# Performance work log

Measured on AMD Instinct MI355X. Metric: run time of the kernel, lower is better.

The kernel has to match this reference:

```python
import jax, jax.numpy as jnp
import numpy as np

B, N, T_FULL, T, KS, FEAT = 32, 360, 512, 64, 8, 8
NLAYERS = 3   # DCGRU layers
GLAYERS = 4   # bidirectional GRU layers in GruKRegion


def _gru_layer(x, Wih, Whh, bih, bhh, reverse):
    # x: [M, Tg, in] -> [M, Tg, H]; PyTorch GRU gate order (r, z, n)
    M = x.shape[0]
    Hh = Whh.shape[1]
    xp = jnp.einsum('mti,gi->mtg', x, Wih) + bih  # precompute input projections
    if reverse:
        xp = xp[:, ::-1]

    def step(h, xg):
        gh = jnp.einsum('mh,gh->mg', h, Whh) + bhh
        xr, xz, xn = jnp.split(xg, 3, -1)
        hr, hz, hn = jnp.split(gh, 3, -1)
        r = jax.nn.sigmoid(xr + hr)
        z = jax.nn.sigmoid(xz + hz)
        n = jnp.tanh(xn + r * hn)
        hnew = (1.0 - z) * n + z * h
        return hnew, hnew

    _, hs = jax.lax.scan(step, jnp.zeros((M, Hh), x.dtype), jnp.swapaxes(xp, 0, 1))
    hs = jnp.swapaxes(hs, 0, 1)
    if reverse:
        hs = hs[:, ::-1]
    return hs


def _dcgru_cell(x, h, adj, gw, gb, cw, cb):
    # x, h: [B, N] (rnn_units = 1); adj: [B, N, N]; max_diffusion_step = 2
    def gconv(inp, st, W, bias):
        x0 = jnp.stack([inp, st], axis=-1)                     # [B,N,2]
        x1 = jnp.einsum('bnm,bmc->bnc', adj, x0)
        x2 = 2.0 * jnp.einsum('bnm,bmc->bnc', adj, x1) - x0    # Chebyshev recurrence
        # torch layout: [B,N,C,num_matrices] flattened channel-major
        xc = jnp.stack([x0, x1, x2], axis=-1).reshape(x0.shape[0], N, 6)
        return jnp.einsum('bnf,fo->bno', xc, W) + bias

    gates = jax.nn.sigmoid(gconv(x, h, gw, gb))                # [B,N,2]
    r, u = gates[..., 0], gates[..., 1]
    c = jnp.tanh(gconv(x, r * h, cw, cb)[..., 0])
    return u * h + (1.0 - u) * c


def _forward(full_seq, reconstruct_seq, node_feas, temperature,
             g0wih, g0whh, g0bih, g0bhh, gwih, gwhh, gbih, gbhh,
             l1w, l1b, l2w, l2b,
             enc_gw, enc_gb, enc_cw, enc_cb,
             dec_gw, dec_gb, dec_cw, dec_cb, proj_w, proj_b):
    b, n, tfull = full_seq.shape
    # ---- GruKRegion feature extractor ----
    x = full_seq.reshape(b * n, tfull // KS, KS)
    out = jnp.concatenate(
        [_gru_layer(x, g0wih[0], g0whh[0], g0bih[0], g0bhh[0], False),
         _gru_layer(x, g0wih[1], g0whh[1], g0bih[1], g0bhh[1], True)], axis=-1)
    for l in range(GLAYERS - 1):
        out = jnp.concatenate(
            [_gru_layer(out, gwih[l, 0], gwhh[l, 0], gbih[l, 0], gbhh[l, 0], False),
             _gru_layer(out, gwih[l, 1], gwhh[l, 1], gbih[l, 1], gbhh[l, 1], True)], axis=-1)
    feat = out[:, -1, :].reshape(b, n, 2 * KS)
    feat = jax.nn.leaky_relu(jnp.einsum('bnf,of->bno', feat, l1w) + l1b, 0.2)
    feat = jnp.einsum('bnf,of->bno', feat, l2w) + l2b          # [B,N,FEAT]
    # ---- Embed2GraphByProduct ----
    logits = jnp.einsum('bjk,bpk->bjp', feat, feat)            # [B,N,N]
    # ---- hard gumbel softmax ----
    U = jax.random.uniform(jax.random.key(42), logits.shape, logits.dtype)
    g = -jnp.log(-jnp.log(U + 1e-10) + 1e-10)
    y_soft = jax.nn.softmax((logits + g) / temperature, axis=-1)
    y_hard = jax.nn.one_hot(jnp.argmax(y_soft, -1), n, dtype=y_soft.dtype)
    adj = y_soft + jax.lax.stop_gradient(y_hard - y_soft)
    adj = jnp.where(jnp.eye(n, dtype=bool), 0.0, adj)          # zero diagonal
    # (original computes a random-walk matrix then discards it; skipped)
    # ---- encoder: scan over time, 3 stacked DCGRU layers ----
    seq = jnp.transpose(reconstruct_seq, (2, 0, 1))            # [T,B,N]

    def enc_step(hid, xt):
        o = xt
        new = []
        for l in range(NLAYERS):
            hnew = _dcgru_cell(o, hid[l], adj, enc_gw[l], enc_gb[l], enc_cw[l], enc_cb[l])
            new.append(hnew)
            o = hnew
        return jnp.stack(new), None

    hid, _ = jax.lax.scan(enc_step, jnp.zeros((NLAYERS, b, n), seq.dtype), seq)

    def dec_step(carry, _):
        hidc, inp = carry
        o = inp
        new = []
        for l in range(NLAYERS):
            hnew = _dcgru_cell(o, hidc[l], adj, dec_gw[l], dec_gb[l], dec_cw[l], dec_cb[l])
            new.append(hnew)
            o = hnew
        proj = o * proj_w[0, 0] + proj_b[0]                    # Linear(1,1)
        return (jnp.stack(new), proj), proj

    _, outs = jax.lax.scan(dec_step, (hid, jnp.zeros((b, n), seq.dtype)), None, length=T)
    return jnp.transpose(outs, (1, 2, 0))                      # [B,N,T]


def setup_inputs():
    key = jax.random.key(0)
    ks = jax.random.split(key, 24)
    s = 0.2
    p = lambda k, sh: jax.random.normal(k, sh, jnp.float32) * s
    return dict(
        full_seq=jax.random.normal(ks[0], (B, N, T_FULL), jnp.float32),
        reconstruct_seq=jax.random.normal(ks[1], (B, N, T), jnp.float32),
        node_feas=jax.random.normal(ks[2], (B, N, KS), jnp.float32),
        temperature=jnp.ones((), jnp.float32),
        g0wih=p(ks[3], (2, 3 * KS, KS)), g0whh=p(ks[4], (2, 3 * KS, KS)),
        g0bih=p(ks[5], (2, 3 * KS)), g0bhh=p(ks[6], (2, 3 * KS)),
        gwih=p(ks[7], (GLAYERS - 1, 2, 3 * KS, 2 * KS)),
        gwhh=p(ks[8], (GLAYERS - 1, 2, 3 * KS, KS)),
        gbih=p(ks[9], (GLAYERS - 1, 2, 3 * KS)), gbhh=p(ks[10], (GLAYERS - 1, 2, 3 * KS)),
        l1w=p(ks[11], (KS, 2 * KS)), l1b=p(ks[12], (KS,)),
        l2w=p(ks[13], (FEAT, KS)), l2b=p(ks[14], (FEAT,)),
        enc_gw=p(ks[15], (NLAYERS, 6, 2)), enc_gb=jnp.ones((NLAYERS, 2), jnp.float32),
        enc_cw=p(ks[16], (NLAYERS, 6, 1)), enc_cb=jnp.zeros((NLAYERS, 1), jnp.float32),
        dec_gw=p(ks[17], (NLAYERS, 6, 2)), dec_gb=jnp.ones((NLAYERS, 2), jnp.float32),
        dec_cw=p(ks[18], (NLAYERS, 6, 1)), dec_cb=jnp.zeros((NLAYERS, 1), jnp.float32),
        proj_w=p(ks[19], (1, 1)), proj_b=jnp.zeros((1,), jnp.float32),
    )


def reference(full_seq, reconstruct_seq, node_feas, temperature,
              g0wih, g0whh, g0bih, g0bhh, gwih, gwhh, gbih, gbhh,
              l1w, l1b, l2w, l2b,
              enc_gw, enc_gb, enc_cw, enc_cb,
              dec_gw, dec_gb, dec_cw, dec_cb, proj_w, proj_b):
    return _forward(full_seq, reconstruct_seq, node_feas, temperature,
                    g0wih, g0whh, g0bih, g0bhh, gwih, gwhh, gbih, gbhh,
                    l1w, l1b, l2w, l2b,
                    enc_gw, enc_gb, enc_cw, enc_cb,
                    dec_gw, dec_gb, dec_cw, dec_cb, proj_w, proj_b)
```

## Files before the change

### kernel.cpp

```cpp
#include <hip/hip_runtime.h>
#include <math.h>

#define M_SEQ 11520
#define NNODE 360
#define NB    32
#define TT    64

__device__ __forceinline__ float fsigd(float x)  { return 1.0f / (1.0f + __expf(-x)); }
__device__ __forceinline__ float ftanhd(float x) { return 1.0f - 2.0f / (__expf(2.0f * x) + 1.0f); }

__device__ __forceinline__ void lds_barrier()
{
    asm volatile("s_waitcnt lgkmcnt(0)" ::: "memory");
    __builtin_amdgcn_sched_barrier(0);
    __builtin_amdgcn_s_barrier();
    __builtin_amdgcn_sched_barrier(0);
}

__device__ __forceinline__ unsigned rotl32(unsigned x, int n) { return (x << n) | (x >> (32 - n)); }

__device__ __forceinline__ void tf2x32(unsigned& x0, unsigned& x1)
{
    const unsigned k0 = 0u, k1 = 42u, k2 = 0u ^ 42u ^ 0x1BD11BDAu;
    x0 += k0; x1 += k1;
#define R4(a,b,c,d) \
    x0 += x1; x1 = rotl32(x1,a); x1 ^= x0; \
    x0 += x1; x1 = rotl32(x1,b); x1 ^= x0; \
    x0 += x1; x1 = rotl32(x1,c); x1 ^= x0; \
    x0 += x1; x1 = rotl32(x1,d); x1 ^= x0;
    R4(13,15,26,6)   x0 += k1; x1 += k2 + 1u;
    R4(17,29,16,24)  x0 += k2; x1 += k0 + 2u;
    R4(13,15,26,6)   x0 += k0; x1 += k1 + 3u;
    R4(17,29,16,24)  x0 += k1; x1 += k2 + 4u;
    R4(13,15,26,6)   x0 += k2; x1 += k0 + 5u;
#undef R4
}

__device__ __forceinline__ float jax_uniform(unsigned idx)
{
    unsigned x0 = 0u, x1 = idx;
    tf2x32(x0, x1);
    unsigned bits = x0 ^ x1;
    return __uint_as_float((bits >> 9) | 0x3f800000u) - 1.0f;
}

template<int K>
__device__ __forceinline__ void swz_fma(float h, const float* w0, const float* w1,
                                        const float* w2, float& g0, float& g1, float& g2)
{
    float hk = __int_as_float(
        __builtin_amdgcn_ds_swizzle(__float_as_int(h), (K << 5) | 0x18));
    g0 += hk * w0[K];
    g1 += hk * w1[K];
    g2 += hk * w2[K];
    if constexpr (K < 7)
        swz_fma<K + 1>(h, w0, w1, w2, g0, g1, g2);
}

template<int I>
__device__ __forceinline__ void ldx(float* __restrict__ xv, const float* __restrict__ p)
{
    const float4* p4 = reinterpret_cast<const float4*>(p);
#pragma unroll
    for (int q = 0; q < I / 4; ++q) {
        float4 f = p4[q];
        xv[4*q] = f.x; xv[4*q+1] = f.y; xv[4*q+2] = f.z; xv[4*q+3] = f.w;
    }
}

template<int I>
__device__ __forceinline__ void xgates(const float* __restrict__ xv,
    const float* wx0, const float* wx1, const float* wx2,
    float bx0, float bx1, float bx2, float& xr, float& xz, float& xn)
{
    xr = bx0; xz = bx1; xn = bx2;
#pragma unroll
    for (int k = 0; k < I; ++k) {
        xr += xv[k] * wx0[k];
        xz += xv[k] * wx1[k];
        xn += xv[k] * wx2[k];
    }
}

__device__ __forceinline__ float hstep(float h, float xr, float xz, float xn,
    const float* w0, const float* w1, const float* w2,
    float bh0, float bh1, float bh2)
{
    float gh0 = bh0, gh1 = bh1, gh2 = bh2;
    swz_fma<0>(h, w0, w1, w2, gh0, gh1, gh2);
    float r  = fsigd(xr + gh0);
    float z  = fsigd(xz + gh1);
    float nn = ftanhd(xn + r * gh2);
    return (1.f - z) * nn + z * h;
}

template<int I, bool LASTONLY>
__global__ __launch_bounds__(256) void gru_fused(
    const float* __restrict__ x,
    const float* __restrict__ wih,
    const float* __restrict__ whh,
    const float* __restrict__ bih,
    const float* __restrict__ bhh,
    float* __restrict__ out)
{
    const int tid = blockIdx.x * 256 + threadIdx.x;
    const int j   = tid & 7;
    const int md  = tid >> 3;
    if (md >= M_SEQ * 2) return;
    const int m = md >> 1, dir = md & 1;

    float wx0[I], wx1[I], wx2[I];
    const float* WI = wih + dir * 24 * I;
#pragma unroll
    for (int k = 0; k < I; ++k) {
        wx0[k] = WI[j * I + k];
        wx1[k] = WI[(8 + j) * I + k];
        wx2[k] = WI[(16 + j) * I + k];
    }
    float w0[8], w1[8], w2[8];
    const float* WH = whh + dir * 192;
#pragma unroll
    for (int k = 0; k < 8; ++k) {
        w0[k] = WH[j * 8 + k];
        w1[k] = WH[(8 + j) * 8 + k];
        w2[k] = WH[(16 + j) * 8 + k];
    }
    const float bx0 = bih[dir*24 + j], bx1 = bih[dir*24 + 8 + j], bx2 = bih[dir*24 + 16 + j];
    const float bh0 = bhh[dir*24 + j], bh1 = bhh[dir*24 + 8 + j], bh2 = bhh[dir*24 + 16 + j];

    const float* xm = x + (size_t)m * TT * I;
    float* om = out + (size_t)m * TT * 16 + dir * 8 + j;

    const int tstep = dir ? -1 : 1;
    const int tbase = dir ? TT - 1 : 0;

    float h = 0.f;
    float xva[I], xvb[I];
    ldx<I>(xva, xm + (tbase) * I);
    ldx<I>(xvb, xm + (tbase + tstep) * I);
    float cr, cz, cn;
    xgates<I>(xva, wx0, wx1, wx2, bx0, bx1, bx2, cr, cz, cn);

    for (int tt = 0; tt < TT; tt += 2) {
        const int t0 = tbase + tstep * tt;
        const int t1 = t0 + tstep;
        if (tt + 2 < TT) ldx<I>(xva, xm + (t0 + 2 * tstep) * I);
        float nr, nz, nn;
        xgates<I>(xvb, wx0, wx1, wx2, bx0, bx1, bx2, nr, nz, nn);
        h = hstep(h, cr, cz, cn, w0, w1, w2, bh0, bh1, bh2);
        if (!LASTONLY || t0 == TT - 1) om[t0 * 16] = h;
        if (tt + 3 < TT) ldx<I>(xvb, xm + (t0 + 3 * tstep) * I);
        h = hstep(h, nr, nz, nn, w0, w1, w2, bh0, bh1, bh2);
        if (!LASTONLY || t1 == TT - 1) om[t1 * 16] = h;
        xgates<I>(xva, wx0, wx1, wx2, bx0, bx1, bx2, cr, cz, cn);
    }
}

__global__ void feat_kernel(const float* __restrict__ gout,
                            const float* __restrict__ l1w, const float* __restrict__ l1b,
                            const float* __restrict__ l2w, const float* __restrict__ l2b,
                            float* __restrict__ feat)
{
    int m = blockIdx.x * blockDim.x + threadIdx.x;
    if (m >= M_SEQ) return;
    const float* xp = gout + (size_t)m * TT * 16 + (TT - 1) * 16;
    float xv[16];
#pragma unroll
    for (int i = 0; i < 16; ++i) xv[i] = xp[i];
    float h1[8];
#pragma unroll
    for (int o = 0; o < 8; ++o) {
        float a = 0.f;
#pragma unroll
        for (int f = 0; f < 16; ++f) a += xv[f] * l1w[o * 16 + f];
        a += l1b[o];
        h1[o] = (a >= 0.f) ? a : 0.2f * a;
    }
#pragma unroll
    for (int o = 0; o < 8; ++o) {
        float a = 0.f;
#pragma unroll
        for (int f = 0; f < 8; ++f) a += h1[f] * l2w[o * 8 + f];
        feat[(size_t)m * 8 + o] = a + l2b[o];
    }
}

__global__ void adj_kernel(const float* __restrict__ feat,
                           const float* __restrict__ tptr,
                           int* __restrict__ colp, float* __restrict__ vp)
{
    const int gw   = (blockIdx.x * blockDim.x + threadIdx.x) >> 6;
    const int lane = threadIdx.x & 63;
    if (gw >= NB * NNODE) return;
    const int b = gw / NNODE;
    const int n = gw - b * NNODE;
    const float T = tptr[0];
    const float* fb = feat + (size_t)b * NNODE * 8;
    float fn[8];
#pragma unroll
    for (int k = 0; k < 8; ++k) fn[k] = fb[(size_t)n * 8 + k];

    float sv[6];
    float mval = -3.0e38f; int midx = 1 << 30;
#pragma unroll
    for (int s = 0; s < 6; ++s) {
        int p = s * 64 + lane;
        float xs = -3.0e38f;
        if (p < NNODE) {
            const float* fp = fb + (size_t)p * 8;
            float d = 0.f;
#pragma unroll
            for (int k = 0; k < 8; ++k) d += fn[k] * fp[k];
            unsigned idx = (unsigned)gw * 360u + (unsigned)p;
            float u   = jax_uniform(idx);
            float gum = -logf(-logf(u + 1e-10f) + 1e-10f);
            xs = (d + gum) / T;
            if (xs > mval) { mval = xs; midx = p; }
        }
        sv[s] = xs;
    }
    for (int off = 32; off > 0; off >>= 1) {
        float ov = __shfl_xor(mval, off);
        int   oi = __shfl_xor(midx, off);
        if (ov > mval || (ov == mval && oi < midx)) { mval = ov; midx = oi; }
    }
    float ssum = 0.f;
#pragma unroll
    for (int s = 0; s < 6; ++s) {
        int p = s * 64 + lane;
        if (p < NNODE) ssum += expf(sv[s] - mval);
    }
    for (int off = 32; off > 0; off >>= 1) ssum += __shfl_xor(ssum, off);
    if (lane == 0) {
        float ys = 1.0f / ssum;
        float v  = ys + (1.0f - ys);
        if (midx == n) v = 0.0f;
        colp[gw] = midx;
        vp[gw]   = v;
    }
}

__device__ __forceinline__ void dc_layer(
    float o_own, float oa, float ob,
    float& hn, float ha, float hb,
    float v, float vv, int c1, int c2, bool act, int n,
    const float* __restrict__ W, float bgr, float bgu,
    const float* __restrict__ C, float cb,
    float* __restrict__ s_rh)
{
    float f1 = v * oa, f2 = vv * ob - o_own;
    float f4 = v * ha, f5 = vv * hb - hn;
    float r  = fsigd(o_own*W[0] + f1*W[2] + f2*W[4] + hn*W[6] + f4*W[8] + f5*W[10] + bgr);
    float rh = r * hn;
    if (act) s_rh[n] = rh;
    lds_barrier();
    float rha = s_rh[c1], rhb = s_rh[c2];
    float u  = fsigd(o_own*W[1] + f1*W[3] + f2*W[5] + hn*W[7] + f4*W[9] + f5*W[11] + bgu);
    float cnd = ftanhd(o_own*C[0] + f1*C[1] + f2*C[2] + rh*C[3]
                       + (v*rha)*C[4] + (vv*rhb - rh)*C[5] + cb);
    hn = u * hn + (1.f - u) * cnd;
}

__global__ __launch_bounds__(384, 1) void decode_kernel(
    const float* __restrict__ rec,
    const int*   __restrict__ colp, const float* __restrict__ vp,
    const float* __restrict__ egw, const float* __restrict__ egb,
    const float* __restrict__ ecw, const float* __restrict__ ecb,
    const float* __restrict__ dgw, const float* __restrict__ dgb,
    const float* __restrict__ dcw, const float* __restrict__ dcb,
    const float* __restrict__ pw,  const float* __restrict__ pb,
    float* __restrict__ outp)
{
    __shared__ float s_h[2][3][NNODE];
    __shared__ float s_x[2][NNODE];
    __shared__ float s_o[NNODE];
    __shared__ float s_rh[NNODE];
    __shared__ float s_v[NNODE];
    __shared__ int   s_c[NNODE];

    const int b = blockIdx.x;
    const int n = threadIdx.x;
    const bool act = n < NNODE;

    float inp0 = 0.f;
    if (act) {
        s_c[n] = colp[b * NNODE + n];
        s_v[n] = vp[b * NNODE + n];
        inp0   = rec[((size_t)b * NNODE + n) * TT + 0];
        s_h[0][0][n] = 0.f; s_h[0][1][n] = 0.f; s_h[0][2][n] = 0.f;
        s_x[0][n] = inp0;
    }
    __syncthreads();

    int c1 = 0, c2 = 0;
    float v = 0.f, vv = 0.f;
    if (act) {
        c1 = s_c[n];
        c2 = s_c[c1];
        v  = s_v[n];
        vv = 2.f * v * s_v[c1];
    }
    const float projw = pw[0], projb = pb[0];
    float hreg[3] = {0.f, 0.f, 0.f};

    float Wg[36], Bg[6], Wc[18], Cb[3];
#pragma unroll
    for (int k = 0; k < 36; ++k) Wg[k] = egw[k];
#pragma unroll
    for (int k = 0; k < 6;  ++k) Bg[k] = egb[k];
#pragma unroll
    for (int k = 0; k < 18; ++k) Wc[k] = ecw[k];
#pragma unroll
    for (int k = 0; k < 3;  ++k) Cb[k] = ecb[k];

    float o_own = inp0;
    int p = 0;
    for (int t = 0; t < TT; ++t) {
        float nx = (act && t + 1 < TT) ? rec[((size_t)b * NNODE + n) * TT + t + 1] : 0.f;
        float xa  = s_x[p][c1],    xb  = s_x[p][c2];
        float h0a = s_h[p][0][c1], h0b = s_h[p][0][c2];
        float h1a = s_h[p][1][c1], h1b = s_h[p][1][c2];
        float h2a = s_h[p][2][c1], h2b = s_h[p][2][c2];
        const int q = p ^ 1;
        dc_layer(o_own, xa, xb, hreg[0], h0a, h0b, v, vv, c1, c2, act, n,
                 Wg, Bg[0], Bg[1], Wc, Cb[0], s_rh);
        if (act) { s_h[q][0][n] = hreg[0]; s_o[n] = hreg[0]; }
        lds_barrier();
        float oa = s_o[c1], ob = s_o[c2];
        dc_layer(hreg[0], oa, ob, hreg[1], h1a, h1b, v, vv, c1, c2, act, n,
                 Wg + 12, Bg[2], Bg[3], Wc + 6, Cb[1], s_rh);
        if (act) { s_h[q][1][n] = hreg[1]; s_o[n] = hreg[1]; }
        lds_barrier();
        oa = s_o[c1]; ob = s_o[c2];
        dc_layer(hreg[1], oa, ob, hreg[2], h2a, h2b, v, vv, c1, c2, act, n,
                 Wg + 24, Bg[4], Bg[5], Wc + 12, Cb[2], s_rh);
        if (act) { s_h[q][2][n] = hreg[2]; s_x[q][n] = nx; }
        lds_barrier();
        o_own = nx; p = q;
    }

#pragma unroll
    for (int k = 0; k < 36; ++k) Wg[k] = dgw[k];
#pragma unroll
    for (int k = 0; k < 6;  ++k) Bg[k] = dgb[k];
#pragma unroll
    for (int k = 0; k < 18; ++k) Wc[k] = dcw[k];
#pragma unroll
    for (int k = 0; k < 3;  ++k) Cb[k] = dcb[k];

    float dinp = 0.f;
    for (int t = 0; t < TT; ++t) {
        float xa  = s_x[p][c1],    xb  = s_x[p][c2];
        float h0a = s_h[p][0][c1], h0b = s_h[p][0][c2];
        float h1a = s_h[p][1][c1], h1b = s_h[p][1][c2];
        float h2a = s_h[p][2][c1], h2b = s_h[p][2][c2];
        const int q = p ^ 1;
        dc_layer(dinp, xa, xb, hreg[0], h0a, h0b, v, vv, c1, c2, act, n,
                 Wg, Bg[0], Bg[1], Wc, Cb[0], s_rh);
        if (act) { s_h[q][0][n] = hreg[0]; s_o[n] = hreg[0]; }
        lds_barrier();
        float oa = s_o[c1], ob = s_o[c2];
        dc_layer(hreg[0], oa, ob, hreg[1], h1a, h1b, v, vv, c1, c2, act, n,
                 Wg + 12, Bg[2], Bg[3], Wc + 6, Cb[1], s_rh);
        if (act) { s_h[q][1][n] = hreg[1]; s_o[n] = hreg[1]; }
        lds_barrier();
        oa = s_o[c1]; ob = s_o[c2];
        dc_layer(hreg[1], oa, ob, hreg[2], h2a, h2b, v, vv, c1, c2, act, n,
                 Wg + 24, Bg[4], Bg[5], Wc + 12, Cb[2], s_rh);
        float proj = hreg[2] * projw + projb;
        if (act) {
            s_h[q][2][n] = hreg[2];
            s_x[q][n] = proj;
            outp[((size_t)b * NNODE + n) * TT + t] = proj;
        }
        lds_barrier();
        dinp = proj; p = q;
    }
}

extern "C" void kernel_launch(void* const* d_in, const int* in_sizes, int n_in,
                              void* d_out, int out_size, void* d_ws, size_t ws_size,
                              hipStream_t stream)
{
    (void)in_sizes; (void)n_in; (void)out_size; (void)ws_size;
    const float* full_seq = (const float*)d_in[0];
    const float* rec_seq  = (const float*)d_in[1];
    const float* temp     = (const float*)d_in[3];
    const float* g0wih    = (const float*)d_in[4];
    const float* g0whh    = (const float*)d_in[5];
    const float* g0bih    = (const float*)d_in[6];
    const float* g0bhh    = (const float*)d_in[7];
    const float* gwih     = (const float*)d_in[8];
    const float* gwhh     = (const float*)d_in[9];
    const float* gbih     = (const float*)d_in[10];
    const float* gbhh     = (const float*)d_in[11];
    const float* l1w      = (const float*)d_in[12];
    const float* l1b      = (const float*)d_in[13];
    const float* l2w      = (const float*)d_in[14];
    const float* l2b      = (const float*)d_in[15];
    const float* enc_gw   = (const float*)d_in[16];
    const float* enc_gb   = (const float*)d_in[17];
    const float* enc_cw   = (const float*)d_in[18];
    const float* enc_cb   = (const float*)d_in[19];
    const float* dec_gw   = (const float*)d_in[20];
    const float* dec_gb   = (const float*)d_in[21];
    const float* dec_cw   = (const float*)d_in[22];
    const float* dec_cb   = (const float*)d_in[23];
    const float* proj_w   = (const float*)d_in[24];
    const float* proj_b   = (const float*)d_in[25];
    float* outp = (float*)d_out;

    float* ws   = (float*)d_ws;
    float* feat = ws;
    float* vbuf = feat + (size_t)M_SEQ * 8;
    int*   cbuf = (int*)(vbuf + M_SEQ);
    float* bufA = (float*)(cbuf + M_SEQ);
    float* bufB = bufA + (size_t)M_SEQ * TT * 16;

    const int ggru = (M_SEQ * 2 * 8) / 256;
    gru_fused<8,false><<<ggru, 256, 0, stream>>>(full_seq, g0wih, g0whh, g0bih, g0bhh, bufA);
    gru_fused<16,false><<<ggru, 256, 0, stream>>>(bufA, gwih + 0 * 768, gwhh + 0 * 384,
                                                  gbih + 0 * 48, gbhh + 0 * 48, bufB);
    gru_fused<16,false><<<ggru, 256, 0, stream>>>(bufB, gwih + 1 * 768, gwhh + 1 * 384,
                                                  gbih + 1 * 48, gbhh + 1 * 48, bufA);
    gru_fused<16,true><<<ggru, 256, 0, stream>>>(bufA, gwih + 2 * 768, gwhh + 2 * 384,
                                                 gbih + 2 * 48, gbhh + 2 * 48, bufB);
    feat_kernel<<<M_SEQ / 256, 256, 0, stream>>>(bufB, l1w, l1b, l2w, l2b, feat);
    adj_kernel<<<(NB * NNODE) / 4, 256, 0, stream>>>(feat, temp, cbuf, vbuf);
    decode_kernel<<<NB, 384, 0, stream>>>(rec_seq, cbuf, vbuf,
                                          enc_gw, enc_gb, enc_cw, enc_cb,
                                          dec_gw, dec_gb, dec_cw, dec_cb,
                                          proj_w, proj_b, outp);
}
```

Measured before the change: 525.6 us.

## Wavefront-pipeline encoder DCGRU layers across two thread groups in decode kernel

The decode kernel now launches 768 threads per block and splits them into two groups of 384. During the encoder, group A computes layer 0 and most of layer 1 for step k while group B finishes layer 1 and computes layer 2 for step k-1. This skewed schedule shortens the serial chain of barrier-separated phases per timestep, since the encoder is latency-bound with only 32 blocks. It costs extra LDS buffers, a staged layer-1 handoff between the groups, and idle B threads during the decoder, which still runs sequentially.

```diff
diff --git a/kernel.cpp b/kernel.cpp
--- a/kernel.cpp
+++ b/kernel.cpp
@@ -241,6 +241,7 @@
 }
 
 __device__ __forceinline__ void dc_layer(
+    bool comp,
     float o_own, float oa, float ob,
     float& hn, float ha, float hb,
     float v, float vv, int c1, int c2, bool act, int n,
@@ -248,20 +249,25 @@
     const float* __restrict__ C, float cb,
     float* __restrict__ s_rh)
 {
-    float f1 = v * oa, f2 = vv * ob - o_own;
-    float f4 = v * ha, f5 = vv * hb - hn;
-    float r  = fsigd(o_own*W[0] + f1*W[2] + f2*W[4] + hn*W[6] + f4*W[8] + f5*W[10] + bgr);
-    float rh = r * hn;
-    if (act) s_rh[n] = rh;
+    float f1 = 0.f, f2 = 0.f, f4 = 0.f, f5 = 0.f, rh = 0.f;
+    if (comp) {
+        f1 = v * oa; f2 = vv * ob - o_own;
+        f4 = v * ha; f5 = vv * hb - hn;
+        float r = fsigd(o_own*W[0] + f1*W[2] + f2*W[4] + hn*W[6] + f4*W[8] + f5*W[10] + bgr);
+        rh = r * hn;
+        if (act) s_rh[n] = rh;
+    }
     lds_barrier();
-    float rha = s_rh[c1], rhb = s_rh[c2];
-    float u  = fsigd(o_own*W[1] + f1*W[3] + f2*W[5] + hn*W[7] + f4*W[9] + f5*W[11] + bgu);
-    float cnd = ftanhd(o_own*C[0] + f1*C[1] + f2*C[2] + rh*C[3]
-                       + (v*rha)*C[4] + (vv*rhb - rh)*C[5] + cb);
-    hn = u * hn + (1.f - u) * cnd;
-}
-
-__global__ __launch_bounds__(384, 1) void decode_kernel(
+    if (comp) {
+        float rha = s_rh[c1], rhb = s_rh[c2];
+        float u  = fsigd(o_own*W[1] + f1*W[3] + f2*W[5] + hn*W[7] + f4*W[9] + f5*W[11] + bgu);
+        float cnd = ftanhd(o_own*C[0] + f1*C[1] + f2*C[2] + rh*C[3]
+                           + (v*rha)*C[4] + (vv*rhb - rh)*C[5] + cb);
+        hn = u * hn + (1.f - u) * cnd;
+    }
+}
+
+__global__ __launch_bounds__(768, 1) void decode_kernel(
     const float* __restrict__ rec,
     const int*   __restrict__ colp, const float* __restrict__ vp,
     const float* __restrict__ egw, const float* __restrict__ egb,
@@ -272,36 +278,47 @@
     float* __restrict__ outp)
 {
     __shared__ float s_h[2][3][NNODE];
-    __shared__ float s_x[2][NNODE];
+    __shared__ float s_xe[2][NNODE];
+    __shared__ float s_r1[2][NNODE];
+    __shared__ float s_u1[2][NNODE];
+    __shared__ float s_c1[2][NNODE];
+    __shared__ float s_rh0[NNODE];
+    __shared__ float s_rh2[NNODE];
     __shared__ float s_o[NNODE];
-    __shared__ float s_rh[NNODE];
+    __shared__ float s_rhd[NNODE];
     __shared__ float s_v[NNODE];
     __shared__ int   s_c[NNODE];
 
-    const int b = blockIdx.x;
-    const int n = threadIdx.x;
-    const bool act = n < NNODE;
-
-    float inp0 = 0.f;
-    if (act) {
-        s_c[n] = colp[b * NNODE + n];
-        s_v[n] = vp[b * NNODE + n];
-        inp0   = rec[((size_t)b * NNODE + n) * TT + 0];
-        s_h[0][0][n] = 0.f; s_h[0][1][n] = 0.f; s_h[0][2][n] = 0.f;
-        s_x[0][n] = inp0;
+    const int  b    = blockIdx.x;
+    const int  tid  = threadIdx.x;
+    const bool isB  = tid >= 384;
+    const bool isA  = !isB;
+    const int  node = isB ? tid - 384 : tid;
+    const bool actN = node < NNODE;
+
+    const float* recb = rec + ((size_t)b * NNODE + node) * TT;
+
+    float o_own = 0.f, xq1 = 0.f;
+    if (isA && actN) {
+        s_c[node] = colp[b * NNODE + node];
+        s_v[node] = vp[b * NNODE + node];
+        o_own = recb[0];
+        xq1   = recb[1];
+        s_xe[0][node] = o_own;
+#pragma unroll
+        for (int l = 0; l < 3; ++l) { s_h[0][l][node] = 0.f; s_h[1][l][node] = 0.f; }
     }
     __syncthreads();
 
     int c1 = 0, c2 = 0;
     float v = 0.f, vv = 0.f;
-    if (act) {
-        c1 = s_c[n];
+    if (actN) {
+        c1 = s_c[node];
         c2 = s_c[c1];
-        v  = s_v[n];
+        v  = s_v[node];
         vv = 2.f * v * s_v[c1];
     }
     const float projw = pw[0], projb = pb[0];
-    float hreg[3] = {0.f, 0.f, 0.f};
 
     float Wg[36], Bg[6], Wc[18], Cb[3];
 #pragma unroll
@@ -313,65 +330,136 @@
 #pragma unroll
     for (int k = 0; k < 3;  ++k) Cb[k] = ecb[k];
 
-    float o_own = inp0;
+    float h0r = 0.f, h1r = 0.f, h2r = 0.f;
+
+    for (int k = 0; k <= TT; ++k) {
+        const int  pk = k & 1, qk = pk ^ 1;
+        const bool aAct = isA && actN && (k < TT);
+        const bool bAct = isB && actN && (k >= 1);
+        float nx2 = 0.f;
+        if (aAct && k + 2 < TT) nx2 = recb[k + 2];
+
+        float fA1=0.f, fA2=0.f, fA4=0.f, fA5=0.f, rhA=0.f;
+        if (isA) {
+            float xa  = s_xe[pk][c1],   xb  = s_xe[pk][c2];
+            float h0a = s_h[pk][0][c1], h0b = s_h[pk][0][c2];
+            fA1 = v * xa;  fA2 = vv * xb - o_own;
+            fA4 = v * h0a; fA5 = vv * h0b - h0r;
+            float rA = fsigd(o_own*Wg[0] + fA1*Wg[2] + fA2*Wg[4] + h0r*Wg[6]
+                             + fA4*Wg[8] + fA5*Wg[10] + Bg[0]);
+            rhA = rA * h0r;
+            if (aAct) s_rh0[node] = rhA;
+        } else {
+            float rh1o = s_r1[pk][node];
+            float rh1a = s_r1[pk][c1], rh1b = s_r1[pk][c2];
+            float u1v  = s_u1[pk][node], cp1v = s_c1[pk][node];
+            float cnd1 = ftanhd(cp1v + rh1o*Wc[9] + (v*rh1a)*Wc[10]
+                                + (vv*rh1b - rh1o)*Wc[11] + Cb[1]);
+            if (bAct) { h1r = u1v * h1r + (1.f - u1v) * cnd1; s_h[qk][1][node] = h1r; }
+        }
+        lds_barrier();
+
+        float fB1=0.f, fB2=0.f, fB4=0.f, fB5=0.f, rhB=0.f;
+        if (isA) {
+            float rh0a = s_rh0[c1], rh0b = s_rh0[c2];
+            float uA = fsigd(o_own*Wg[1] + fA1*Wg[3] + fA2*Wg[5] + h0r*Wg[7]
+                             + fA4*Wg[9] + fA5*Wg[11] + Bg[1]);
+            float cndA = ftanhd(o_own*Wc[0] + fA1*Wc[1] + fA2*Wc[2] + rhA*Wc[3]
+                                + (v*rh0a)*Wc[4] + (vv*rh0b - rhA)*Wc[5] + Cb[0]);
+            if (aAct) {
+                h0r = uA * h0r + (1.f - uA) * cndA;
+                s_h[qk][0][node] = h0r;
+                s_xe[qk][node]   = xq1;
+            }
+        } else {
+            float o2a = s_h[qk][1][c1], o2b = s_h[qk][1][c2];
+            float h2a = s_h[pk][2][c1], h2b = s_h[pk][2][c2];
+            fB1 = v * o2a; fB2 = vv * o2b - h1r;
+            fB4 = v * h2a; fB5 = vv * h2b - h2r;
+            float rB = fsigd(h1r*Wg[24] + fB1*Wg[26] + fB2*Wg[28] + h2r*Wg[30]
+                             + fB4*Wg[32] + fB5*Wg[34] + Bg[4]);
+            rhB = rB * h2r;
+            if (bAct) s_rh2[node] = rhB;
+        }
+        lds_barrier();
+
+        if (isA) {
+            float o1a = s_h[qk][0][c1], o1b = s_h[qk][0][c2];
+            float h1own = s_h[qk][1][node];
+            float h1a = s_h[qk][1][c1], h1b = s_h[qk][1][c2];
+            float fC1 = v * o1a, fC2 = vv * o1b - h0r;
+            float fC4 = v * h1a, fC5 = vv * h1b - h1own;
+            float r1 = fsigd(h0r*Wg[12] + fC1*Wg[14] + fC2*Wg[16] + h1own*Wg[18]
+                             + fC4*Wg[20] + fC5*Wg[22] + Bg[2]);
+            float u1 = fsigd(h0r*Wg[13] + fC1*Wg[15] + fC2*Wg[17] + h1own*Wg[19]
+                             + fC4*Wg[21] + fC5*Wg[23] + Bg[3]);
+            float cp1 = h0r*Wc[6] + fC1*Wc[7] + fC2*Wc[8];
+            if (aAct) { s_r1[qk][node] = r1 * h1own; s_u1[qk][node] = u1; s_c1[qk][node] = cp1; }
+        } else {
+            float rh2a = s_rh2[c1], rh2b = s_rh2[c2];
+            float u2 = fsigd(h1r*Wg[25] + fB1*Wg[27] + fB2*Wg[29] + h2r*Wg[31]
+                             + fB4*Wg[33] + fB5*Wg[35] + Bg[5]);
+            float cnd2 = ftanhd(h1r*Wc[12] + fB1*Wc[13] + fB2*Wc[14] + rhB*Wc[15]
+                                + (v*rh2a)*Wc[16] + (vv*rh2b - rhB)*Wc[17] + Cb[2]);
+            if (bAct) { h2r = u2 * h2r + (1.f - u2) * cnd2; s_h[qk][2][node] = h2r; }
+        }
+        lds_barrier();
+        if (isA) { o_own = xq1; xq1 = nx2; }
+    }
+
+    if (tid < NNODE) {
+        s_h[0][1][tid] = s_h[1][1][tid];
+        s_h[0][2][tid] = s_h[1][2][tid];
+        s_xe[0][tid]   = 0.f;
+    }
+    __syncthreads();
+
+    const bool actd = (isA && actN);
+    const int  nd   = actN ? node : 0;
+    float hreg[3];
+    hreg[0] = h0r;
+    hreg[1] = s_h[0][1][nd];
+    hreg[2] = s_h[0][2][nd];
+
+#pragma unroll
+    for (int k = 0; k < 36; ++k) Wg[k] = dgw[k];
+#pragma unroll
+    for (int k = 0; k < 6;  ++k) Bg[k] = dgb[k];
+#pragma unroll
+    for (int k = 0; k < 18; ++k) Wc[k] = dcw[k];
+#pragma unroll
+    for (int k = 0; k < 3;  ++k) Cb[k] = dcb[k];
+
+    float dinp = 0.f;
     int p = 0;
     for (int t = 0; t < TT; ++t) {
-        float nx = (act && t + 1 < TT) ? rec[((size_t)b * NNODE + n) * TT + t + 1] : 0.f;
-        float xa  = s_x[p][c1],    xb  = s_x[p][c2];
-        float h0a = s_h[p][0][c1], h0b = s_h[p][0][c2];
-        float h1a = s_h[p][1][c1], h1b = s_h[p][1][c2];
-        float h2a = s_h[p][2][c1], h2b = s_h[p][2][c2];
+        float xa=0.f, xb=0.f;
+        float h0a=0.f,h0b=0.f,h1a=0.f,h1b=0.f,h2a=0.f,h2b=0.f;
+        if (isA) {
+            xa  = s_xe[p][c1];     xb  = s_xe[p][c2];
+            h0a = s_h[p][0][c1];   h0b = s_h[p][0][c2];
+            h1a = s_h[p][1][c1];   h1b = s_h[p][1][c2];
+            h2a = s_h[p][2][c1];   h2b = s_h[p][2][c2];
+        }
         const int q = p ^ 1;
-        dc_layer(o_own, xa, xb, hreg[0], h0a, h0b, v, vv, c1, c2, act, n,
-                 Wg, Bg[0], Bg[1], Wc, Cb[0], s_rh);
-        if (act) { s_h[q][0][n] = hreg[0]; s_o[n] = hreg[0]; }
+        dc_layer(isA, dinp, xa, xb, hreg[0], h0a, h0b, v, vv, c1, c2, actd, node,
+                 Wg, Bg[0], Bg[1], Wc, Cb[0], s_rhd);
+        if (actd) { s_h[q][0][node] = hreg[0]; s_o[node] = hreg[0]; }
         lds_barrier();
-        float oa = s_o[c1], ob = s_o[c2];
-        dc_layer(hreg[0], oa, ob, hreg[1], h1a, h1b, v, vv, c1, c2, act, n,
-                 Wg + 12, Bg[2], Bg[3], Wc + 6, Cb[1], s_rh);
-        if (act) { s_h[q][1][n] = hreg[1]; s_o[n] = hreg[1]; }
+        float oa=0.f, ob=0.f;
+        if (isA) { oa = s_o[c1]; ob = s_o[c2]; }
+        dc_layer(isA, hreg[0], oa, ob, hreg[1], h1a, h1b, v, vv, c1, c2, actd, node,
+                 Wg + 12, Bg[2], Bg[3], Wc + 6, Cb[1], s_rhd);
+        if (actd) { s_h[q][1][node] = hreg[1]; s_o[node] = hreg[1]; }
         lds_barrier();
-        oa = s_o[c1]; ob = s_o[c2];
-        dc_layer(hreg[1], oa, ob, hreg[2], h2a, h2b, v, vv, c1, c2, act, n,
-                 Wg + 24, Bg[4], Bg[5], Wc + 12, Cb[2], s_rh);
-        if (act) { s_h[q][2][n] = hreg[2]; s_x[q][n] = nx; }
-        lds_barrier();
-        o_own = nx; p = q;
-    }
-
-#pragma unroll
-    for (int k = 0; k < 36; ++k) Wg[k] = dgw[k];
-#pragma unroll
-    for (int k = 0; k < 6;  ++k) Bg[k] = dgb[k];
-#pragma unroll
-    for (int k = 0; k < 18; ++k) Wc[k] = dcw[k];
-#pragma unroll
-    for (int k = 0; k < 3;  ++k) Cb[k] = dcb[k];
-
-    float dinp = 0.f;
-    for (int t = 0; t < TT; ++t) {
-        float xa  = s_x[p][c1],    xb  = s_x[p][c2];
-        float h0a = s_h[p][0][c1], h0b = s_h[p][0][c2];
-        float h1a = s_h[p][1][c1], h1b = s_h[p][1][c2];
-        float h2a = s_h[p][2][c1], h2b = s_h[p][2][c2];
-        const int q = p ^ 1;
-        dc_layer(dinp, xa, xb, hreg[0], h0a, h0b, v, vv, c1, c2, act, n,
-                 Wg, Bg[0], Bg[1], Wc, Cb[0], s_rh);
-        if (act) { s_h[q][0][n] = hreg[0]; s_o[n] = hreg[0]; }
-        lds_barrier();
-        float oa = s_o[c1], ob = s_o[c2];
-        dc_layer(hreg[0], oa, ob, hreg[1], h1a, h1b, v, vv, c1, c2, act, n,
-                 Wg + 12, Bg[2], Bg[3], Wc + 6, Cb[1], s_rh);
-        if (act) { s_h[q][1][n] = hreg[1]; s_o[n] = hreg[1]; }
-        lds_barrier();
-        oa = s_o[c1]; ob = s_o[c2];
-        dc_layer(hreg[1], oa, ob, hreg[2], h2a, h2b, v, vv, c1, c2, act, n,
-                 Wg + 24, Bg[4], Bg[5], Wc + 12, Cb[2], s_rh);
+        if (isA) { oa = s_o[c1]; ob = s_o[c2]; }
+        dc_layer(isA, hreg[1], oa, ob, hreg[2], h2a, h2b, v, vv, c1, c2, actd, node,
+                 Wg + 24, Bg[4], Bg[5], Wc + 12, Cb[2], s_rhd);
         float proj = hreg[2] * projw + projb;
-        if (act) {
-            s_h[q][2][n] = hreg[2];
-            s_x[q][n] = proj;
-            outp[((size_t)b * NNODE + n) * TT + t] = proj;
+        if (actd) {
+            s_h[q][2][node] = hreg[2];
+            s_xe[q][node]   = proj;
+            outp[((size_t)b * NNODE + node) * TT + t] = proj;
         }
         lds_barrier();
         dinp = proj; p = q;
@@ -427,7 +515,7 @@
                                                  gbih + 2 * 48, gbhh + 2 * 48, bufB);
     feat_kernel<<<M_SEQ / 256, 256, 0, stream>>>(bufB, l1w, l1b, l2w, l2b, feat);
     adj_kernel<<<(NB * NNODE) / 4, 256, 0, stream>>>(feat, temp, cbuf, vbuf);
-    decode_kernel<<<NB, 384, 0, stream>>>(rec_seq, cbuf, vbuf,
+    decode_kernel<<<NB, 768, 0, stream>>>(rec_seq, cbuf, vbuf,
                                           enc_gw, enc_gb, enc_cw, enc_cb,
                                           dec_gw, dec_gb, dec_cw, dec_cb,
                                           proj_w, proj_b, outp);
```

After: 512.7 us. -2.5%, faster.
